# Kernel optimization log

Measured on AMD Instinct MI355X. Metric: run time of the kernel, lower is better.

The kernel has to match this reference:

```python
import jax, jax.numpy as jnp
import numpy as np

TIME_STEP = 3  # init_kwargs time_step
D = 512       # input_dim
N = 1024      # node_num
B = 16        # batch


def setup_inputs() -> dict:
    key = jax.random.key(0)
    ks = jax.random.split(key, 16)
    x = jax.random.normal(ks[0], (B, N, D), dtype=jnp.float32)
    # adjacency in [0,1), scaled by 1/N so repeated propagation stays well-conditioned
    in_matrix = jax.random.uniform(ks[1], (N, N), dtype=jnp.float32) / N
    out_matrix = jax.random.uniform(ks[2], (N, N), dtype=jnp.float32) / N
    s = 0.02
    w3w = jax.random.normal(ks[3], (D, 2 * D), dtype=jnp.float32) * s
    b3w = jnp.zeros((D,), dtype=jnp.float32)
    w3u = jax.random.normal(ks[4], (D, D), dtype=jnp.float32) * s
    b3u = jnp.zeros((D,), dtype=jnp.float32)
    w4w = jax.random.normal(ks[5], (D, 2 * D), dtype=jnp.float32) * s
    b4w = jnp.zeros((D,), dtype=jnp.float32)
    w5w = jax.random.normal(ks[6], (D, 2 * D), dtype=jnp.float32) * s
    b5w = jnp.zeros((D,), dtype=jnp.float32)
    w5u = jax.random.normal(ks[7], (D, D), dtype=jnp.float32) * s
    b5u = jnp.zeros((D,), dtype=jnp.float32)
    return {"x": x, "in_matrix": in_matrix, "out_matrix": out_matrix,
            "w3w": w3w, "b3w": b3w, "w3u": w3u, "b3u": b3u,
            "w4w": w4w, "b4w": b4w, "w5w": w5w, "b5w": b5w,
            "w5u": w5u, "b5u": b5u}


def reference(x, in_matrix, out_matrix, w3w, b3w, w3u, b3u, w4w, b4w, w5w, b5w, w5u, b5u):
    # x: [B, N, D]; in/out_matrix: [N, N] (shared across batch, as in torch repeat)
    nodes = x
    for _ in range(TIME_STEP):
        a_in = jnp.einsum('mn,bnd->bmd', in_matrix, nodes)   # [B,N,D]
        a_out = jnp.einsum('mn,bnd->bmd', out_matrix, nodes)  # [B,N,D]
        av = jnp.concatenate([a_in, a_out], axis=-1)           # [B,N,2D]
        f = nodes
        u3 = jnp.einsum('bnd,ed->bne', f, w3u) + b3u           # shared eq3_u term
        zv = jax.nn.sigmoid(jnp.einsum('bnc,ec->bne', av, w3w) + b3w + u3)
        # NOTE: original code reuses fc_eq3_u inside rv (faithful reproduction)
        rv = jax.nn.sigmoid(jnp.einsum('bnc,ec->bne', av, w4w) + b4w + u3)
        hv = jnp.tanh(jnp.einsum('bnc,ec->bne', av, w5w) + b5w
                      + jnp.einsum('bnd,ed->bne', rv * f, w5u) + b5u)
        nodes = (1.0 - zv) * f + zv * hv  # dropout p=0 -> identity
    return (nodes, in_matrix)
```

## Files before the change

kernel.cpp:

```cpp
#include <hip/hip_runtime.h>
#include <cstdint>
#include <cstddef>


#define B_ 16
#define N_ 1024
#define D_ 512
#define S_ (B_ * N_)
#define TWO_D 1024

typedef __attribute__((ext_vector_type(8))) short short8;
typedef __attribute__((ext_vector_type(4))) short s16x4;
typedef __attribute__((ext_vector_type(4))) float f32x4;

#define EPI_AVU3 0
#define EPI_BIG  2
#define EPI_G4   3

__device__ __forceinline__ float bf2f(short u) {
  union { unsigned int i; float f; } v;
  v.i = ((unsigned int)(unsigned short)u) << 16;
  return v.f;
}
__device__ __forceinline__ short f2bf(float f) {
  union { float f; unsigned int i; } v;
  v.f = f;
  unsigned int x = v.i;
  unsigned int r = (x + 0x7fffu + ((x >> 16) & 1u)) >> 16;
  return (short)(unsigned short)r;
}
__device__ __forceinline__ float fast_sigmoid(float x) {
  return __builtin_amdgcn_rcpf(1.f + __expf(-x));
}
__device__ __forceinline__ float fast_tanh(float x) {
  const float t = __expf(-2.f * fabsf(x));
  const float th = (1.f - t) * __builtin_amdgcn_rcpf(1.f + t);
  return __builtin_copysignf(th, x);
}

__device__ __forceinline__ void gload16(const void* g, void* l) {
  __builtin_amdgcn_global_load_lds(
      (__attribute__((address_space(1))) void*)g,
      (__attribute__((address_space(3))) void*)l, 16, 0, 0);
}

template <int EPI>
__global__ __launch_bounds__(512, 4) void gemm_nt(
    const short* A, const short* A2, int lda,
    const short* Bw, const short* Bw2, const short* Bw3, int ldb, int Kin,
    const float* bias0, const float* bias1, const float* bias2,
    const short* u3, const short* fcur,
    const short* hvp, const short* zvp,
    short* out0, short* out1, short* out2,
    float* outf, int twoC) {
  __shared__ __align__(16) short lds_a0[128 * 32];
  __shared__ __align__(16) short lds_b0[128 * 32];
  __shared__ __align__(16) short lds_a1[128 * 32];
  __shared__ __align__(16) short lds_b1[128 * 32];

  const int tid = threadIdx.x;
  const int lane = tid & 63;
  const int wave = tid >> 6;
  const int wr = wave >> 2;
  const int wc = wave & 3;

  int bx = blockIdx.x, by = blockIdx.y, bz = blockIdx.z;
  if constexpr (EPI == EPI_AVU3) {
    const int total = gridDim.x * gridDim.y * gridDim.z;
    const int id = (bz * gridDim.y + by) * gridDim.x + bx;
    if ((total & 7) == 0) {
      const int a = id & 7, m = id >> 3;
      const int l = a * (total >> 3) + m;
      bx = l & 3;
      by = (l >> 2) & 7;
      bz = l >> 5;
    }
  } else {
    const int gx = gridDim.x, gy = gridDim.y;
    if ((gy & 7) == 0) {
      const int id = by * gx + bx;
      const int a = id & 7;
      const int m = id >> 3;
      const int per = gy >> 3;
      by = a * per + m / gx;
      bx = m % gx;
    }
  }

  int m0 = by * 128;
  const int n0 = bx * 128;
  int K = Kin;

  const short* Aeff = A;
  const short* Beff = Bw;
  int lda_e = lda, ldb_e = ldb;
  int nb0 = n0;
  bool isU3 = false;
  int b_ = 0, j_ = 0;
  if constexpr (EPI == EPI_AVU3) {
    if (bz < twoC) {
      b_ = bz >> 1;
      j_ = bz & 1;
      Aeff = j_ ? A2 : A;
      Beff = Bw + (size_t)b_ * ((size_t)D_ * N_);
      lda_e = N_; ldb_e = N_; K = N_;
    } else {
      isU3 = true;
      const int b = bz - twoC;
      Aeff = u3  + (size_t)b * N_ * D_;
      Beff = Bw3 ;
      lda_e = D_; ldb_e = D_; K = D_;
      b_ = b;
    }
  } else if constexpr (EPI == EPI_BIG) {
    if (n0 < 512) { Beff = Bw; nb0 = n0; }
    else if (n0 < 1024) { Beff = Bw2; nb0 = n0 - 512; }
    else { Beff = Bw3; nb0 = n0 - 1024; }
  }

  f32x4 acc[4][2];
#pragma unroll
  for (int i = 0; i < 4; i++)
#pragma unroll
    for (int j = 0; j < 2; j++) acc[i][j] = (f32x4){0.f, 0.f, 0.f, 0.f};

  const int ar = tid >> 2;
  const int sc = tid & 3;
  const int qg = (sc - (ar >> 1)) & 3;
  const int ac = qg * 8;
  char* la0p = (char*)lds_a0 + tid * 16;
  char* lb0p = (char*)lds_b0 + tid * 16;
  char* la1p = (char*)lds_a1 + tid * 16;
  char* lb1p = (char*)lds_b1 + tid * 16;
  const short* ga0 = Aeff + (size_t)(m0 + ar) * lda_e + ac;
  const short* gb0 = Beff + (size_t)(nb0 + ar) * ldb_e + ac;

  const int lm = lane & 15;
  const int qq = lane >> 4;

  int offA[4], offB[2];
#pragma unroll
  for (int i = 0; i < 4; i++) {
    const int Ra = wr * 64 + i * 16 + lm;
    offA[i] = Ra * 64 + (((qq + (Ra >> 1)) & 3) << 4);
  }
#pragma unroll
  for (int j = 0; j < 2; j++) {
    const int Rb = wc * 32 + j * 16 + lm;
    offB[j] = Rb * 64 + (((qq + (Rb >> 1)) & 3) << 4);
  }

#define COMPUTE_TILE(LA, LB)                                                 \
  do {                                                                       \
    short8 af[4], bfr[2];                                                    \
    _Pragma("unroll") for (int i = 0; i < 4; i++)                            \
        af[i] = *(const short8*)((const char*)(LA) + offA[i]);               \
    _Pragma("unroll") for (int j = 0; j < 2; j++)                            \
        bfr[j] = *(const short8*)((const char*)(LB) + offB[j]);              \
    _Pragma("unroll") for (int i = 0; i < 4; i++)                            \
        _Pragma("unroll") for (int j = 0; j < 2; j++)                        \
            acc[i][j] = __builtin_amdgcn_mfma_f32_16x16x32_bf16(             \
                af[i], bfr[j], acc[i][j], 0, 0, 0);                          \
  } while (0)

  gload16(ga0, la0p);
  gload16(gb0, lb0p);
  __syncthreads();

  for (int k0 = 0; k0 < K; k0 += 64) {
    gload16(ga0 + k0 + 32, la1p);
    gload16(gb0 + k0 + 32, lb1p);
    COMPUTE_TILE(lds_a0, lds_b0);
    __syncthreads();

    if (k0 + 64 < K) {
      gload16(ga0 + k0 + 64, la0p);
      gload16(gb0 + k0 + 64, lb0p);
    }
    COMPUTE_TILE(lds_a1, lds_b1);
    __syncthreads();
  }
#undef COMPUTE_TILE

  const int r0 = (lane >> 4) * 4;
#pragma unroll
  for (int i = 0; i < 4; i++) {
#pragma unroll
    for (int j = 0; j < 2; j++) {
#pragma unroll
      for (int r = 0; r < 4; r++) {
        const int grow = m0 + wr * 64 + i * 16 + r0 + r;
        const int gcol = n0 + wc * 32 + j * 16 + lm;
        const float v = acc[i][j][r];
        if constexpr (EPI == EPI_AVU3) {
          if (!isU3) {
            out0[((size_t)(b_ * N_ + grow)) * TWO_D + j_ * D_ + gcol] =
                f2bf(v);
          } else {
            out1[((size_t)(b_ * N_ + grow)) * D_ + gcol] =
                f2bf(v + bias0[gcol]);
          }
        } else if constexpr (EPI == EPI_BIG) {
          if (gcol < 512) {
            const size_t sidx = (size_t)grow * D_ + gcol;
            const float x = v + bias0[gcol] + bf2f(u3[sidx]);
            out0[sidx] = f2bf(fast_sigmoid(x));
          } else if (gcol < 1024) {
            const int e = gcol - 512;
            const size_t sidx = (size_t)grow * D_ + e;
            const float x = v + bias1[e] + bf2f(u3[sidx]);
            out1[sidx] = f2bf(fast_sigmoid(x) * bf2f(fcur[sidx]));
          } else {
            const int e = gcol - 1024;
            const size_t sidx = (size_t)grow * D_ + e;
            out2[sidx] = f2bf(v + bias2[e]);
          }
        } else {
          const size_t sidx = (size_t)grow * D_ + gcol;
          const float x = bf2f(hvp[sidx]) + v + bias0[gcol];
          const float hv = fast_tanh(x);
          const float z = bf2f(zvp[sidx]);
          const float f = bf2f(fcur[sidx]);
          const float res = (1.f - z) * f + z * hv;
          if (outf) outf[sidx] = res;
          else out0[sidx] = f2bf(res);
        }
      }
    }
  }
}

__global__ void transpose_bnd(const short* __restrict__ in,
                              short* __restrict__ out) {
  __shared__ short tile[32][33];
  const int b = blockIdx.z;
  const int n0 = blockIdx.y * 32;
  const int d0 = blockIdx.x * 32;
  const int tx = threadIdx.x, ty = threadIdx.y;
  const short* ip = in + (size_t)b * N_ * D_;
  short* op = out + (size_t)b * N_ * D_;
#pragma unroll
  for (int yy = ty; yy < 32; yy += 8)
    tile[yy][tx] = ip[(size_t)(n0 + yy) * D_ + d0 + tx];
  __syncthreads();
#pragma unroll
  for (int yy = ty; yy < 32; yy += 8)
    op[(size_t)(d0 + yy) * N_ + n0 + tx] = tile[tx][yy];
}

struct CvtJobs {
  const float* src[8];
  short* dst[8];
  int end4[8];
  int tot4;
};
__global__ void cvt_all(CvtJobs j) {
  for (int idx = blockIdx.x * 256 + threadIdx.x; idx < j.tot4;
       idx += gridDim.x * 256) {
    int k = 0, start = 0;
#pragma unroll
    for (int t = 0; t < 8; t++) {
      if (idx >= j.end4[t]) { k = t + 1; start = j.end4[t]; }
    }
    const int rel = idx - start;
    const f32x4 v = ((const f32x4*)j.src[k])[rel];
    s16x4 o;
#pragma unroll
    for (int r = 0; r < 4; r++) o[r] = f2bf(v[r]);
    ((s16x4*)j.dst[k])[rel] = o;
  }
}

extern "C" void kernel_launch(void* const* d_in, const int* in_sizes, int n_in,
                              void* d_out, int out_size, void* d_ws,
                              size_t ws_size, hipStream_t stream) {
  const float* x = (const float*)d_in[0];
  const float* inM = (const float*)d_in[1];
  const float* outM = (const float*)d_in[2];
  const float* w3w = (const float*)d_in[3];
  const float* b3w = (const float*)d_in[4];
  const float* w3u = (const float*)d_in[5];
  const float* b3u = (const float*)d_in[6];
  const float* w4w = (const float*)d_in[7];
  const float* b4w = (const float*)d_in[8];
  const float* w5w = (const float*)d_in[9];
  const float* b5w = (const float*)d_in[10];
  const float* w5u = (const float*)d_in[11];
  const float* b5u = (const float*)d_in[12];
  float* outF = (float*)d_out;

  char* ws = (char*)d_ws;
  size_t off = 0;
  auto alloc = [&](size_t elems) {
    short* p = (short*)(ws + off);
    off = (off + elems * 2 + 255) & ~(size_t)255;
    return p;
  };
  short* nodes = alloc((size_t)S_ * D_);
  short* inMb = alloc((size_t)N_ * N_);
  short* outMb = alloc((size_t)N_ * N_);
  short* w3wb = alloc((size_t)512 * 1024);
  short* w4wb = alloc((size_t)512 * 1024);
  short* w5wb = alloc((size_t)512 * 1024);
  short* w3ub = alloc((size_t)D_ * D_);
  short* w5ub = alloc((size_t)D_ * D_);
  const size_t fixed = off;

  int C = 1;
  for (int c = 16; c >= 1; c >>= 1) {
    const size_t need = fixed + (size_t)7 * c * N_ * D_ * 2 + 8 * 256;
    if (need <= ws_size) { C = c; break; }
  }
  short* T = alloc((size_t)C * D_ * N_);
  short* av = alloc((size_t)C * N_ * TWO_D);
  short* u3 = alloc((size_t)C * N_ * D_);
  short* zv = alloc((size_t)C * N_ * D_);
  short* rf = alloc((size_t)C * N_ * D_);
  short* hvp = alloc((size_t)C * N_ * D_);

  CvtJobs cj;
  const int xs4 = S_ * D_ / 4, nn4 = N_ * N_ / 4;
  const int dd4 = D_ * D_ / 4, wd4 = 512 * 1024 / 4;
  const float* srcs[8] = {x, inM, outM, w3w, w4w, w5w, w3u, w5u};
  short* dsts[8] = {nodes, inMb, outMb, w3wb, w4wb, w5wb, w3ub, w5ub};
  const int lens[8] = {xs4, nn4, nn4, wd4, wd4, wd4, dd4, dd4};
  int cum = 0;
  for (int i = 0; i < 8; i++) {
    cj.src[i] = srcs[i];
    cj.dst[i] = dsts[i];
    cum += lens[i];
    cj.end4[i] = cum;
  }
  cj.tot4 = cum;
  cvt_all<<<1536, 256, 0, stream>>>(cj);
  hipMemcpyAsync(outF + (size_t)S_ * D_, inM, (size_t)N_ * N_ * 4,
                 hipMemcpyDeviceToDevice, stream);

  const dim3 tb32(32, 8);
  const dim3 tg(D_ / 32, N_ / 32, C);
  const dim3 g_avu3(D_ / 128, N_ / 128, 3 * C);
  const dim3 g_d(D_ / 128, C * N_ / 128, 1);
  const dim3 g_big(1536 / 128, C * N_ / 128, 1);

  const int nchunks = B_ / C;
  for (int c = 0; c < nchunks; ++c) {
    short* nodes_c = nodes + (size_t)c * C * N_ * D_;
    float* outF_c = outF + (size_t)c * C * N_ * D_;
    for (int step = 0; step < 3; ++step) {
      transpose_bnd<<<tg, tb32, 0, stream>>>(nodes_c, T);
      gemm_nt<EPI_AVU3><<<g_avu3, 512, 0, stream>>>(
          inMb, outMb, N_, T, nullptr, w3ub, N_, N_, b3u, nullptr, nullptr,
          nodes_c, nullptr, nullptr, nullptr, av, u3, nullptr, nullptr,
          2 * C);
      gemm_nt<EPI_BIG><<<g_big, 512, 0, stream>>>(
          av, nullptr, TWO_D, w3wb, w4wb, w5wb, TWO_D, TWO_D, b3w, b4w, b5w,
          u3, nodes_c, nullptr, nullptr, zv, rf, hvp, nullptr, 0);
      float* outf = (step == 2) ? outF_c : nullptr;
      gemm_nt<EPI_G4><<<g_d, 512, 0, stream>>>(
          rf, nullptr, D_, w5ub, nullptr, nullptr, D_, D_, b5u, nullptr,
          nullptr, nullptr, nodes_c, hvp, zv, nodes_c, nullptr, nullptr,
          outf, 0);
    }
  }
}
```

Baseline: 636.8 us.

## Triple-buffer LDS tiles in GEMM mainloop with explicit vmcnt waits

Replaces the double-buffered K loop with a three-stage LDS ring buffer. Loads are issued two tiles ahead, and explicit s_waitcnt vmcnt counts replace the full __syncthreads drain, so more global-to-LDS traffic can be in flight during the MFMAs. It also lowers the launch_bounds occupancy hint from 4 to 3 to pay for the extra 16KB of LDS per block, which trades occupancy for pipeline depth. The manual vmcnt counts depend on exact load ordering, so correctness rests on the compiler not reordering the loads.

```diff
diff --git a/kernel.cpp b/kernel.cpp
--- a/kernel.cpp
+++ b/kernel.cpp
@@ -44,8 +44,12 @@
       (__attribute__((address_space(3))) void*)l, 16, 0, 0);
 }
 
+#define WAITV(N) asm volatile("s_waitcnt vmcnt(" #N ")" ::: "memory")
+#define BAR() __builtin_amdgcn_s_barrier()
+#define SCHEDB() __builtin_amdgcn_sched_barrier(0)
+
 template <int EPI>
-__global__ __launch_bounds__(512, 4) void gemm_nt(
+__global__ __launch_bounds__(512, 3) void gemm_nt(
     const short* A, const short* A2, int lda,
     const short* Bw, const short* Bw2, const short* Bw3, int ldb, int Kin,
     const float* bias0, const float* bias1, const float* bias2,
@@ -57,6 +61,8 @@
   __shared__ __align__(16) short lds_b0[128 * 32];
   __shared__ __align__(16) short lds_a1[128 * 32];
   __shared__ __align__(16) short lds_b1[128 * 32];
+  __shared__ __align__(16) short lds_a2[128 * 32];
+  __shared__ __align__(16) short lds_b2[128 * 32];
 
   const int tid = threadIdx.x;
   const int lane = tid & 63;
@@ -128,10 +134,19 @@
   const int sc = tid & 3;
   const int qg = (sc - (ar >> 1)) & 3;
   const int ac = qg * 8;
-  char* la0p = (char*)lds_a0 + tid * 16;
-  char* lb0p = (char*)lds_b0 + tid * 16;
-  char* la1p = (char*)lds_a1 + tid * 16;
-  char* lb1p = (char*)lds_b1 + tid * 16;
+  char* wa0 = (char*)lds_a0 + tid * 16;
+  char* wb0 = (char*)lds_b0 + tid * 16;
+  char* wa1 = (char*)lds_a1 + tid * 16;
+  char* wb1 = (char*)lds_b1 + tid * 16;
+  char* wa2 = (char*)lds_a2 + tid * 16;
+  char* wb2 = (char*)lds_b2 + tid * 16;
+  const char* ca0 = (const char*)lds_a0;
+  const char* cb0 = (const char*)lds_b0;
+  const char* ca1 = (const char*)lds_a1;
+  const char* cb1 = (const char*)lds_b1;
+  const char* ca2 = (const char*)lds_a2;
+  const char* cb2 = (const char*)lds_b2;
+
   const short* ga0 = Aeff + (size_t)(m0 + ar) * lda_e + ac;
   const short* gb0 = Beff + (size_t)(nb0 + ar) * ldb_e + ac;
 
@@ -154,33 +169,50 @@
   do {                                                                       \
     short8 af[4], bfr[2];                                                    \
     _Pragma("unroll") for (int i = 0; i < 4; i++)                            \
-        af[i] = *(const short8*)((const char*)(LA) + offA[i]);               \
+        af[i] = *(const short8*)((LA) + offA[i]);                            \
     _Pragma("unroll") for (int j = 0; j < 2; j++)                            \
-        bfr[j] = *(const short8*)((const char*)(LB) + offB[j]);              \
+        bfr[j] = *(const short8*)((LB) + offB[j]);                           \
     _Pragma("unroll") for (int i = 0; i < 4; i++)                            \
         _Pragma("unroll") for (int j = 0; j < 2; j++)                        \
             acc[i][j] = __builtin_amdgcn_mfma_f32_16x16x32_bf16(             \
                 af[i], bfr[j], acc[i][j], 0, 0, 0);                          \
   } while (0)
 
-  gload16(ga0, la0p);
-  gload16(gb0, lb0p);
-  __syncthreads();
-
-  for (int k0 = 0; k0 < K; k0 += 64) {
-    gload16(ga0 + k0 + 32, la1p);
-    gload16(gb0 + k0 + 32, lb1p);
-    COMPUTE_TILE(lds_a0, lds_b0);
-    __syncthreads();
-
-    if (k0 + 64 < K) {
-      gload16(ga0 + k0 + 64, la0p);
-      gload16(gb0 + k0 + 64, lb0p);
-    }
-    COMPUTE_TILE(lds_a1, lds_b1);
-    __syncthreads();
-  }
+#define ROTATE()                                                             \
+  do {                                                                       \
+    char* t1;                                                                \
+    t1 = wa0; wa0 = wa1; wa1 = wa2; wa2 = t1;                                \
+    t1 = wb0; wb0 = wb1; wb1 = wb2; wb2 = t1;                                \
+    const char* t2;                                                          \
+    t2 = ca0; ca0 = ca1; ca1 = ca2; ca2 = t2;                                \
+    t2 = cb0; cb0 = cb1; cb1 = cb2; cb2 = t2;                                \
+  } while (0)
+
+  gload16(ga0 + 0, wa0);  gload16(gb0 + 0, wb0);
+  gload16(ga0 + 32, wa1); gload16(gb0 + 32, wb1);
+  gload16(ga0 + 64, wa2); gload16(gb0 + 64, wb2);
+
+  int k0 = 0;
+  for (; k0 + 96 < K; k0 += 32) {
+    WAITV(4);
+    BAR();
+    COMPUTE_TILE(ca0, cb0);
+    BAR();
+    SCHEDB();
+    gload16(ga0 + k0 + 96, wa0);
+    gload16(gb0 + k0 + 96, wb0);
+    ROTATE();
+  }
+  WAITV(4); BAR();
+  COMPUTE_TILE(ca0, cb0);
+  BAR(); ROTATE();
+  WAITV(2); BAR();
+  COMPUTE_TILE(ca0, cb0);
+  BAR(); ROTATE();
+  WAITV(0); BAR();
+  COMPUTE_TILE(ca0, cb0);
 #undef COMPUTE_TILE
+#undef ROTATE
 
   const int r0 = (lane >> 4) * 4;
 #pragma unroll
```

After: 653.6 us. +2.6%, slower.

## Enlarge GEMM block tile to 256x128 with 64x64 per-wave subtiles

Applied to the files above, without the earlier changes.

Doubles the GEMM block tile in M from 128 to 256 and reorganizes the eight waves into a 4x2 grid of 64x64 subtiles, each holding a 4x4 MFMA accumulator array. The goal is more operand reuse per LDS read and per global load, with fewer blocks. The A loads are split into two 128-row halves, the XOR-style LDS swizzle is dropped in favour of plain row-major offsets, and the grid shapes and AVU3 block remapping are adjusted. This doubles accumulator registers while raising the launch_bounds occupancy hint, which risks register spills. The unswizzled LDS layout also risks bank conflicts, and the smaller grid may underfill the CUs.

```diff
diff --git a/kernel.cpp b/kernel.cpp
--- a/kernel.cpp
+++ b/kernel.cpp
@@ -45,7 +45,7 @@
 }
 
 template <int EPI>
-__global__ __launch_bounds__(512, 4) void gemm_nt(
+__global__ __launch_bounds__(512, 6) void gemm_nt(
     const short* A, const short* A2, int lda,
     const short* Bw, const short* Bw2, const short* Bw3, int ldb, int Kin,
     const float* bias0, const float* bias1, const float* bias2,
@@ -53,16 +53,16 @@
     const short* hvp, const short* zvp,
     short* out0, short* out1, short* out2,
     float* outf, int twoC) {
-  __shared__ __align__(16) short lds_a0[128 * 32];
+  __shared__ __align__(16) short lds_a0[256 * 32];
   __shared__ __align__(16) short lds_b0[128 * 32];
-  __shared__ __align__(16) short lds_a1[128 * 32];
+  __shared__ __align__(16) short lds_a1[256 * 32];
   __shared__ __align__(16) short lds_b1[128 * 32];
 
   const int tid = threadIdx.x;
   const int lane = tid & 63;
   const int wave = tid >> 6;
-  const int wr = wave >> 2;
-  const int wc = wave & 3;
+  const int wm = wave >> 1;
+  const int wn = wave & 1;
 
   int bx = blockIdx.x, by = blockIdx.y, bz = blockIdx.z;
   if constexpr (EPI == EPI_AVU3) {
@@ -72,8 +72,8 @@
       const int a = id & 7, m = id >> 3;
       const int l = a * (total >> 3) + m;
       bx = l & 3;
-      by = (l >> 2) & 7;
-      bz = l >> 5;
+      by = (l >> 2) & 3;
+      bz = l >> 4;
     }
   } else {
     const int gx = gridDim.x, gy = gridDim.y;
@@ -87,7 +87,7 @@
     }
   }
 
-  int m0 = by * 128;
+  int m0 = by * 256;
   const int n0 = bx * 128;
   int K = Kin;
 
@@ -118,79 +118,81 @@
     else { Beff = Bw3; nb0 = n0 - 1024; }
   }
 
-  f32x4 acc[4][2];
+  f32x4 acc[4][4];
 #pragma unroll
   for (int i = 0; i < 4; i++)
 #pragma unroll
-    for (int j = 0; j < 2; j++) acc[i][j] = (f32x4){0.f, 0.f, 0.f, 0.f};
-
-  const int ar = tid >> 2;
-  const int sc = tid & 3;
-  const int qg = (sc - (ar >> 1)) & 3;
-  const int ac = qg * 8;
-  char* la0p = (char*)lds_a0 + tid * 16;
-  char* lb0p = (char*)lds_b0 + tid * 16;
-  char* la1p = (char*)lds_a1 + tid * 16;
-  char* lb1p = (char*)lds_b1 + tid * 16;
-  const short* ga0 = Aeff + (size_t)(m0 + ar) * lda_e + ac;
-  const short* gb0 = Beff + (size_t)(nb0 + ar) * ldb_e + ac;
+    for (int j = 0; j < 4; j++) acc[i][j] = (f32x4){0.f, 0.f, 0.f, 0.f};
+
+  const int srow = tid >> 2;
+  const int skoff = (tid & 3) * 8;
+  const short* gA0 = Aeff + (size_t)(m0 + srow) * lda_e + skoff;
+  const short* gA1 = Aeff + (size_t)(m0 + 128 + srow) * lda_e + skoff;
+  const short* gB0 = Beff + (size_t)(nb0 + srow) * ldb_e + skoff;
+  char* const da0_0 = (char*)lds_a0 + tid * 16;
+  char* const da0_1 = (char*)lds_a0 + 8192 + tid * 16;
+  char* const db0_0 = (char*)lds_b0 + tid * 16;
+  char* const da1_0 = (char*)lds_a1 + tid * 16;
+  char* const da1_1 = (char*)lds_a1 + 8192 + tid * 16;
+  char* const db1_0 = (char*)lds_b1 + tid * 16;
 
   const int lm = lane & 15;
   const int qq = lane >> 4;
-
-  int offA[4], offB[2];
-#pragma unroll
-  for (int i = 0; i < 4; i++) {
-    const int Ra = wr * 64 + i * 16 + lm;
-    offA[i] = Ra * 64 + (((qq + (Ra >> 1)) & 3) << 4);
-  }
-#pragma unroll
-  for (int j = 0; j < 2; j++) {
-    const int Rb = wc * 32 + j * 16 + lm;
-    offB[j] = Rb * 64 + (((qq + (Rb >> 1)) & 3) << 4);
-  }
+  int offA[4], offB[4];
+#pragma unroll
+  for (int i = 0; i < 4; i++)
+    offA[i] = (wm * 64 + i * 16 + lm) * 64 + qq * 16;
+#pragma unroll
+  for (int j = 0; j < 4; j++)
+    offB[j] = (wn * 64 + j * 16 + lm) * 64 + qq * 16;
+
+#define STAGE0(kk) do { \
+    gload16(gA0 + (kk), da0_0); \
+    gload16(gA1 + (kk), da0_1); \
+    gload16(gB0 + (kk), db0_0); } while (0)
+#define STAGE1(kk) do { \
+    gload16(gA0 + (kk), da1_0); \
+    gload16(gA1 + (kk), da1_1); \
+    gload16(gB0 + (kk), db1_0); } while (0)
 
 #define COMPUTE_TILE(LA, LB)                                                 \
   do {                                                                       \
-    short8 af[4], bfr[2];                                                    \
+    short8 af[4], bfr[4];                                                    \
     _Pragma("unroll") for (int i = 0; i < 4; i++)                            \
         af[i] = *(const short8*)((const char*)(LA) + offA[i]);               \
-    _Pragma("unroll") for (int j = 0; j < 2; j++)                            \
+    _Pragma("unroll") for (int j = 0; j < 4; j++)                            \
         bfr[j] = *(const short8*)((const char*)(LB) + offB[j]);              \
     _Pragma("unroll") for (int i = 0; i < 4; i++)                            \
-        _Pragma("unroll") for (int j = 0; j < 2; j++)                        \
+        _Pragma("unroll") for (int j = 0; j < 4; j++)                        \
             acc[i][j] = __builtin_amdgcn_mfma_f32_16x16x32_bf16(             \
                 af[i], bfr[j], acc[i][j], 0, 0, 0);                          \
   } while (0)
 
-  gload16(ga0, la0p);
-  gload16(gb0, lb0p);
+  STAGE0(0);
   __syncthreads();
 
   for (int k0 = 0; k0 < K; k0 += 64) {
-    gload16(ga0 + k0 + 32, la1p);
-    gload16(gb0 + k0 + 32, lb1p);
+    STAGE1(k0 + 32);
     COMPUTE_TILE(lds_a0, lds_b0);
     __syncthreads();
 
-    if (k0 + 64 < K) {
-      gload16(ga0 + k0 + 64, la0p);
-      gload16(gb0 + k0 + 64, lb0p);
-    }
+    if (k0 + 64 < K) STAGE0(k0 + 64);
     COMPUTE_TILE(lds_a1, lds_b1);
     __syncthreads();
   }
 #undef COMPUTE_TILE
-
-  const int r0 = (lane >> 4) * 4;
+#undef STAGE0
+#undef STAGE1
+
+  const int r4 = lane >> 4;
 #pragma unroll
   for (int i = 0; i < 4; i++) {
 #pragma unroll
-    for (int j = 0; j < 2; j++) {
+    for (int j = 0; j < 4; j++) {
 #pragma unroll
       for (int r = 0; r < 4; r++) {
-        const int grow = m0 + wr * 64 + i * 16 + r0 + r;
-        const int gcol = n0 + wc * 32 + j * 16 + lm;
+        const int grow = m0 + wm * 64 + i * 16 + r4 * 4 + r;
+        const int gcol = n0 + wn * 64 + j * 16 + lm;
         const float v = acc[i][j][r];
         if constexpr (EPI == EPI_AVU3) {
           if (!isU3) {
@@ -338,9 +340,9 @@
 
   const dim3 tb32(32, 8);
   const dim3 tg(D_ / 32, N_ / 32, C);
-  const dim3 g_avu3(D_ / 128, N_ / 128, 3 * C);
-  const dim3 g_d(D_ / 128, C * N_ / 128, 1);
-  const dim3 g_big(1536 / 128, C * N_ / 128, 1);
+  const dim3 g_avu3(D_ / 128, N_ / 256, 3 * C);
+  const dim3 g_d(D_ / 128, C * N_ / 256, 1);
+  const dim3 g_big(1536 / 128, C * N_ / 256, 1);
 
   const int nchunks = B_ / C;
   for (int c = 0; c < nchunks; ++c) {
```

Result: slower. 1.952 ms (+206.6%).

## Replace big gate GEMM with 256x256 eight-phase pipelined MFMA kernel

Applied to the files above, without the earlier changes.

Adds a dedicated kernel for the av×[W3w;W4w;W5w] GEMM. It uses 256x256 output tiles, a 64-wide K step and eight LDS buffers staged with async global-to-LDS loads, interleaved with MFMA quadrants under setprio and explicit waitcnt/barriers. It also swizzles the block ordering across groups of eight for cache locality. The goal is more data reuse per tile and better overlap of loads with math than the 128x128 generic kernel, at the cost of heavy LDS use (128KB) and an occupancy of one block per CU.

```diff
diff --git a/kernel.cpp b/kernel.cpp
--- a/kernel.cpp
+++ b/kernel.cpp
@@ -42,6 +42,222 @@
   __builtin_amdgcn_global_load_lds(
       (__attribute__((address_space(1))) void*)g,
       (__attribute__((address_space(3))) void*)l, 16, 0, 0);
+}
+
+#define WAITV(N) asm volatile("s_waitcnt vmcnt(" #N ")" ::: "memory")
+#define BAR() __builtin_amdgcn_s_barrier()
+#define SCHEDB() __builtin_amdgcn_sched_barrier(0)
+
+__global__ __launch_bounds__(512) void gemm_big_8ph(
+    const short* A, const short* Bw, const short* Bw2, const short* Bw3,
+    const float* bias0, const float* bias1, const float* bias2,
+    const short* u3, const short* fcur,
+    short* out0, short* out1, short* out2) {
+  __shared__ __align__(16) short sA00[8192];
+  __shared__ __align__(16) short sA01[8192];
+  __shared__ __align__(16) short sB00[8192];
+  __shared__ __align__(16) short sB01[8192];
+  __shared__ __align__(16) short sA10[8192];
+  __shared__ __align__(16) short sA11[8192];
+  __shared__ __align__(16) short sB10[8192];
+  __shared__ __align__(16) short sB11[8192];
+
+  const int tid = threadIdx.x;
+  const int lane = tid & 63;
+  const int wave = tid >> 6;
+  const int wm = wave & 3;
+  const int wn = wave >> 2;
+
+  int bx = blockIdx.x, by = blockIdx.y;
+  {
+    const int gx = gridDim.x, gy = gridDim.y;
+    if ((gy & 7) == 0) {
+      const int id = by * gx + bx;
+      const int a = id & 7;
+      const int m = id >> 3;
+      const int per = gy >> 3;
+      by = a * per + m / gx;
+      bx = m % gx;
+    }
+  }
+  const int m0 = by * 256;
+  const int n0 = bx * 256;
+
+  const short* Beff;
+  int nb0;
+  if (n0 < 512) { Beff = Bw; nb0 = n0; }
+  else if (n0 < 1024) { Beff = Bw2; nb0 = n0 - 512; }
+  else { Beff = Bw3; nb0 = n0 - 1024; }
+
+  f32x4 acc[2][2][2][4];
+#pragma unroll
+  for (int R = 0; R < 2; R++)
+#pragma unroll
+    for (int Cq = 0; Cq < 2; Cq++)
+#pragma unroll
+      for (int fm = 0; fm < 2; fm++)
+#pragma unroll
+        for (int fn = 0; fn < 4; fn++)
+          acc[R][Cq][fm][fn] = (f32x4){0.f, 0.f, 0.f, 0.f};
+
+  const int rr = tid >> 3;
+  const int qv = ((tid & 7) ^ (rr & 7)) * 8;
+  const short* pA00 = A + (size_t)(m0 + rr) * TWO_D + qv;
+  const short* pA01 = A + (size_t)(m0 + 64 + rr) * TWO_D + qv;
+  const short* pA10 = A + (size_t)(m0 + 128 + rr) * TWO_D + qv;
+  const short* pA11 = A + (size_t)(m0 + 192 + rr) * TWO_D + qv;
+  const short* pB00 = Beff + (size_t)(nb0 + rr) * TWO_D + qv;
+  const short* pB01 = Beff + (size_t)(nb0 + 64 + rr) * TWO_D + qv;
+  const short* pB10 = Beff + (size_t)(nb0 + 128 + rr) * TWO_D + qv;
+  const short* pB11 = Beff + (size_t)(nb0 + 192 + rr) * TWO_D + qv;
+  const int dst0 = tid * 16;
+  const int dst1 = 8192 + tid * 16;
+
+#define STAGE_A0(ARR, kn) do { \
+    gload16(pA00 + (size_t)(kn) * 64, (char*)ARR + dst0); \
+    gload16(pA01 + (size_t)(kn) * 64, (char*)ARR + dst1); } while (0)
+#define STAGE_A1(ARR, kn) do { \
+    gload16(pA10 + (size_t)(kn) * 64, (char*)ARR + dst0); \
+    gload16(pA11 + (size_t)(kn) * 64, (char*)ARR + dst1); } while (0)
+#define STAGE_B0(ARR, kn) do { \
+    gload16(pB00 + (size_t)(kn) * 64, (char*)ARR + dst0); \
+    gload16(pB01 + (size_t)(kn) * 64, (char*)ARR + dst1); } while (0)
+#define STAGE_B1(ARR, kn) do { \
+    gload16(pB10 + (size_t)(kn) * 64, (char*)ARR + dst0); \
+    gload16(pB11 + (size_t)(kn) * 64, (char*)ARR + dst1); } while (0)
+
+  const int lm = lane & 15;
+  const int qq = lane >> 4;
+  int offA[2][2], offB[4][2];
+#pragma unroll
+  for (int fm = 0; fm < 2; fm++)
+#pragma unroll
+    for (int ks = 0; ks < 2; ks++) {
+      const int rw = wm * 32 + fm * 16 + lm;
+      offA[fm][ks] = rw * 128 + (((ks * 4 + qq) ^ (lm & 7)) << 4);
+    }
+#pragma unroll
+  for (int fn = 0; fn < 4; fn++)
+#pragma unroll
+    for (int ks = 0; ks < 2; ks++) {
+      const int rw = wn * 64 + fn * 16 + lm;
+      offB[fn][ks] = rw * 128 + (((ks * 4 + qq) ^ (lm & 7)) << 4);
+    }
+
+  short8 a0f[2][2], a1f[2][2], b_f[4][2];
+
+#define READ_A(dst, ARR) \
+  _Pragma("unroll") for (int fm = 0; fm < 2; fm++) \
+  _Pragma("unroll") for (int ks = 0; ks < 2; ks++) \
+      dst[fm][ks] = *(const short8*)((const char*)ARR + offA[fm][ks]);
+#define READ_B(ARR) \
+  _Pragma("unroll") for (int fn = 0; fn < 4; fn++) \
+  _Pragma("unroll") for (int ks = 0; ks < 2; ks++) \
+      b_f[fn][ks] = *(const short8*)((const char*)ARR + offB[fn][ks]);
+#define MFMA_Q(R, Cq, AF) \
+  SCHEDB(); BAR(); \
+  __builtin_amdgcn_s_setprio(1); \
+  _Pragma("unroll") for (int fm = 0; fm < 2; fm++) \
+  _Pragma("unroll") for (int fn = 0; fn < 4; fn++) \
+  _Pragma("unroll") for (int ks = 0; ks < 2; ks++) \
+      acc[R][Cq][fm][fn] = __builtin_amdgcn_mfma_f32_16x16x32_bf16( \
+          AF[fm][ks], b_f[fn][ks], acc[R][Cq][fm][fn], 0, 0, 0); \
+  __builtin_amdgcn_s_setprio(0); SCHEDB()
+
+  const int KT = TWO_D >> 6;
+
+  STAGE_A0(sA00, 0);
+  STAGE_B0(sB00, 0);
+  STAGE_A1(sA01, 0);
+  STAGE_B1(sB01, 0);
+  STAGE_B0(sB10, 1);
+  STAGE_A1(sA11, 1);
+  WAITV(4); BAR();
+
+  for (int k = 0; k < KT / 2 - 1; ++k) {
+    const int t = 2 * k;
+    READ_A(a0f, sA00); READ_B(sB00);
+    STAGE_A0(sA10, t + 1);
+    MFMA_Q(0, 0, a0f); BAR();
+    READ_A(a1f, sA01);
+    STAGE_B1(sB11, t + 1);
+    MFMA_Q(1, 0, a1f); BAR();
+    READ_B(sB01);
+    STAGE_B0(sB00, t + 2);
+    MFMA_Q(1, 1, a1f); BAR();
+    STAGE_A1(sA01, t + 2);
+    MFMA_Q(0, 1, a0f); WAITV(4); BAR();
+    READ_A(a0f, sA10); READ_B(sB10);
+    STAGE_A0(sA00, t + 2);
+    MFMA_Q(0, 0, a0f); BAR();
+    READ_A(a1f, sA11);
+    STAGE_B1(sB01, t + 2);
+    MFMA_Q(1, 0, a1f); BAR();
+    READ_B(sB11);
+    STAGE_B0(sB10, t + 3);
+    MFMA_Q(1, 1, a1f); BAR();
+    STAGE_A1(sA11, t + 3);
+    MFMA_Q(0, 1, a0f); WAITV(4); BAR();
+  }
+  {
+    READ_A(a0f, sA00); READ_B(sB00);
+    STAGE_A0(sA10, KT - 1);
+    MFMA_Q(0, 0, a0f); BAR();
+    READ_A(a1f, sA01);
+    STAGE_B1(sB11, KT - 1);
+    MFMA_Q(1, 0, a1f); BAR();
+    READ_B(sB01);
+    MFMA_Q(1, 1, a1f); BAR();
+    MFMA_Q(0, 1, a0f); WAITV(0); BAR();
+    READ_A(a0f, sA10); READ_B(sB10);
+    MFMA_Q(0, 0, a0f); BAR();
+    READ_A(a1f, sA11);
+    MFMA_Q(1, 0, a1f); BAR();
+    READ_B(sB11);
+    MFMA_Q(1, 1, a1f); BAR();
+    MFMA_Q(0, 1, a0f);
+  }
+#undef MFMA_Q
+#undef READ_A
+#undef READ_B
+#undef STAGE_A0
+#undef STAGE_A1
+#undef STAGE_B0
+#undef STAGE_B1
+
+  const int r4 = lane >> 4;
+#pragma unroll
+  for (int R = 0; R < 2; R++) {
+#pragma unroll
+    for (int Cq = 0; Cq < 2; Cq++) {
+#pragma unroll
+      for (int fm = 0; fm < 2; fm++) {
+#pragma unroll
+        for (int fn = 0; fn < 4; fn++) {
+#pragma unroll
+          for (int r = 0; r < 4; r++) {
+            const int grow = m0 + R * 128 + wm * 32 + fm * 16 + r4 * 4 + r;
+            const int gcol = n0 + Cq * 128 + wn * 64 + fn * 16 + lm;
+            const float v = acc[R][Cq][fm][fn][r];
+            if (gcol < 512) {
+              const size_t sidx = (size_t)grow * D_ + gcol;
+              const float x = v + bias0[gcol] + bf2f(u3[sidx]);
+              out0[sidx] = f2bf(fast_sigmoid(x));
+            } else if (gcol < 1024) {
+              const int e = gcol - 512;
+              const size_t sidx = (size_t)grow * D_ + e;
+              const float x = v + bias1[e] + bf2f(u3[sidx]);
+              out1[sidx] = f2bf(fast_sigmoid(x) * bf2f(fcur[sidx]));
+            } else {
+              const int e = gcol - 1024;
+              const size_t sidx = (size_t)grow * D_ + e;
+              out2[sidx] = f2bf(v + bias2[e]);
+            }
+          }
+        }
+      }
+    }
+  }
 }
 
 template <int EPI>
@@ -112,10 +328,6 @@
       lda_e = D_; ldb_e = D_; K = D_;
       b_ = b;
     }
-  } else if constexpr (EPI == EPI_BIG) {
-    if (n0 < 512) { Beff = Bw; nb0 = n0; }
-    else if (n0 < 1024) { Beff = Bw2; nb0 = n0 - 512; }
-    else { Beff = Bw3; nb0 = n0 - 1024; }
   }
 
   f32x4 acc[4][2];
@@ -199,21 +411,6 @@
           } else {
             out1[((size_t)(b_ * N_ + grow)) * D_ + gcol] =
                 f2bf(v + bias0[gcol]);
-          }
-        } else if constexpr (EPI == EPI_BIG) {
-          if (gcol < 512) {
-            const size_t sidx = (size_t)grow * D_ + gcol;
-            const float x = v + bias0[gcol] + bf2f(u3[sidx]);
-            out0[sidx] = f2bf(fast_sigmoid(x));
-          } else if (gcol < 1024) {
-            const int e = gcol - 512;
-            const size_t sidx = (size_t)grow * D_ + e;
-            const float x = v + bias1[e] + bf2f(u3[sidx]);
-            out1[sidx] = f2bf(fast_sigmoid(x) * bf2f(fcur[sidx]));
-          } else {
-            const int e = gcol - 1024;
-            const size_t sidx = (size_t)grow * D_ + e;
-            out2[sidx] = f2bf(v + bias2[e]);
           }
         } else {
           const size_t sidx = (size_t)grow * D_ + gcol;
@@ -340,7 +537,7 @@
   const dim3 tg(D_ / 32, N_ / 32, C);
   const dim3 g_avu3(D_ / 128, N_ / 128, 3 * C);
   const dim3 g_d(D_ / 128, C * N_ / 128, 1);
-  const dim3 g_big(1536 / 128, C * N_ / 128, 1);
+  const dim3 g_big8(1536 / 256, C * N_ / 256, 1);
 
   const int nchunks = B_ / C;
   for (int c = 0; c < nchunks; ++c) {
@@ -352,9 +549,9 @@
           inMb, outMb, N_, T, nullptr, w3ub, N_, N_, b3u, nullptr, nullptr,
           nodes_c, nullptr, nullptr, nullptr, av, u3, nullptr, nullptr,
           2 * C);
-      gemm_nt<EPI_BIG><<<g_big, 512, 0, stream>>>(
-          av, nullptr, TWO_D, w3wb, w4wb, w5wb, TWO_D, TWO_D, b3w, b4w, b5w,
-          u3, nodes_c, nullptr, nullptr, zv, rf, hvp, nullptr, 0);
+      gemm_big_8ph<<<g_big8, 512, 0, stream>>>(
+          av, w3wb, w4wb, w5wb, b3w, b4w, b5w,
+          u3, nodes_c, zv, rf, hvp);
       float* outf = (step == 2) ? outF_c : nullptr;
       gemm_nt<EPI_G4><<<g_d, 512, 0, stream>>>(
           rf, nullptr, D_, w5ub, nullptr, nullptr, D_, D_, b5u, nullptr,
```

Measured after the change: 790.6 us. 24.2% more time.
